# Kernel optimization log

Hardware: AMD Instinct MI355X
Metric: run time of the kernel (lower is better)

## Reference

```python
import jax, jax.numpy as jnp
import numpy as np

PADDED_NODE_ID = -1


def setup_inputs() -> dict:
    key = jax.random.key(0)
    k0, k1, k2, k3 = jax.random.split(key, 4)
    B, N, F = 1024, 512, 64
    src_ids = jax.random.randint(k0, (B, N), 0, 1000, dtype=jnp.int64 if jax.config.jax_enable_x64 else jnp.int32)
    dst_ids = jax.random.randint(k1, (B, N), 0, 1000, dtype=src_ids.dtype)
    W1 = jax.random.normal(k2, (1, F), dtype=jnp.float32) * 0.1   # Linear(1 -> F)
    b1 = jnp.zeros((F,), dtype=jnp.float32)
    W2 = jax.random.normal(k3, (F, F), dtype=jnp.float32) * 0.05  # Linear(F -> F)
    b2 = jnp.zeros((F,), dtype=jnp.float32)
    return {"src_ids": src_ids, "dst_ids": dst_ids, "W1": W1, "b1": b1, "W2": W2, "b2": b2}


def _count_freqs(src_ids, dst_ids):
    # For each row, count occurrences of each neighbor id within its own row
    # and within the paired row (cross-lookup). Equivalent to np.unique counts
    # plus dict-based cross mapping in the original, vectorized as pairwise
    # equality reductions over [B, N, N].
    def eq_count(a, b):
        return (a[:, :, None] == b[:, None, :]).sum(-1).astype(jnp.float32)  # [B, N]

    src_in_src = eq_count(src_ids, src_ids)
    src_in_dst = eq_count(src_ids, dst_ids)
    dst_in_dst = eq_count(dst_ids, dst_ids)
    dst_in_src = eq_count(dst_ids, src_ids)

    source_freq = jnp.stack([src_in_src, src_in_dst], axis=-1)  # [B, N, 2]
    dst_freq = jnp.stack([dst_in_dst, dst_in_src], axis=-1)     # [B, N, 2]

    # zero out padded positions
    source_freq = jnp.where((src_ids == PADDED_NODE_ID)[..., None], 0.0, source_freq)
    dst_freq = jnp.where((dst_ids == PADDED_NODE_ID)[..., None], 0.0, dst_freq)
    return source_freq, dst_freq


def reference(src_ids, dst_ids, W1, b1, W2, b2):
    source_freq, dst_freq = _count_freqs(src_ids, dst_ids)  # [B, N, 2] each

    def encode(freq):
        # freq[..., None] has shape [B, N, 2, 1]; Linear(1->F) is an outer product
        h = jax.nn.relu(freq[..., None] * W1[0] + b1)        # [B, N, 2, F]
        h = jnp.einsum('bnkf,fg->bnkg', h, W2) + b2          # [B, N, 2, F]
        return h.sum(axis=2)                                 # [B, N, F]

    return encode(source_freq), encode(dst_freq)
```

## Files before the change

### kernel.cpp

```cpp
#include <hip/hip_runtime.h>

#define BATCH 1024
#define NSEQ  512
#define NF    64
#define TBL_N (NSEQ + 1)
#define HIST_BINS 1024

#define TBL_BLOCKS ((TBL_N + 3) / 4)

__global__ __launch_bounds__(256) void build_table_kernel(
        const float* __restrict__ W1,
        const float* __restrict__ b1,
        const float* __restrict__ W2,
        const float* __restrict__ b2,
        float* __restrict__ tbl) {
    const int c = blockIdx.x * 4 + (threadIdx.x >> 6);
    const int g = threadIdx.x & 63;
    if (c >= TBL_N) return;
    const float cf = (float)c;
    float acc = b2[g];
#pragma unroll 8
    for (int f = 0; f < NF; ++f) {
        float h = fmaxf(cf * W1[f] + b1[f], 0.0f);
        acc += h * W2[f * NF + g];
    }
    tbl[c * NF + g] = acc;
}

__global__ __launch_bounds__(256) void expand_kernel(
        const int* __restrict__ src_ids,
        const int* __restrict__ dst_ids,
        const float* __restrict__ tbl,
        float* __restrict__ out) {
    __shared__ int     s_src[NSEQ];
    __shared__ int     s_dst[NSEQ];
    __shared__ int     hist_s[HIST_BINS];
    __shared__ int     hist_d[HIST_BINS];
    __shared__ ushort2 s_cnt[NSEQ];

    const int t     = threadIdx.x;
    const int which = blockIdx.x & 1;
    const int row   = blockIdx.x >> 1;

#pragma unroll
    for (int i = t; i < HIST_BINS; i += 256) { hist_s[i] = 0; hist_d[i] = 0; }
#pragma unroll
    for (int i = t; i < NSEQ; i += 256) {
        s_src[i] = src_ids[(size_t)row * NSEQ + i];
        s_dst[i] = dst_ids[(size_t)row * NSEQ + i];
    }
    __syncthreads();

#pragma unroll
    for (int i = t; i < NSEQ; i += 256) {
        int si = s_src[i], di = s_dst[i];
        if (si >= 0) atomicAdd(&hist_s[si], 1);
        if (di >= 0) atomicAdd(&hist_d[di], 1);
    }
    __syncthreads();

#pragma unroll
    for (int i = t; i < NSEQ; i += 256) {
        int id = (which == 0) ? s_src[i] : s_dst[i];
        ushort2 c;
        if (id >= 0) {
            c.x = (unsigned short)((which == 0) ? hist_s[id] : hist_d[id]);
            c.y = (unsigned short)((which == 0) ? hist_d[id] : hist_s[id]);
        } else {
            c.x = 0; c.y = 0;
        }
        s_cnt[i] = c;
    }
    __syncthreads();

    const float4* __restrict__ tbl4 = (const float4*)tbl;
    float4* __restrict__ o = (float4*)(out + ((size_t)which * BATCH + row) * NSEQ * NF);
    const int NV = NSEQ * NF / 4;
#pragma unroll 8
    for (int e = t; e < NV; e += 256) {
        int n  = e >> 4;
        int f4 = e & 15;
        ushort2 c = s_cnt[n];
        float4 a0 = tbl4[((int)c.x << 4) + f4];
        float4 a1 = tbl4[((int)c.y << 4) + f4];
        o[e] = make_float4(a0.x + a1.x, a0.y + a1.y, a0.z + a1.z, a0.w + a1.w);
    }
}

extern "C" void kernel_launch(void* const* d_in, const int* in_sizes, int n_in,
                              void* d_out, int out_size, void* d_ws, size_t ws_size,
                              hipStream_t stream) {
    const int*   src_ids = (const int*)d_in[0];
    const int*   dst_ids = (const int*)d_in[1];
    const float* W1 = (const float*)d_in[2];
    const float* b1 = (const float*)d_in[3];
    const float* W2 = (const float*)d_in[4];
    const float* b2 = (const float*)d_in[5];

    float* out = (float*)d_out;
    float* tbl = (float*)d_ws;

    build_table_kernel<<<TBL_BLOCKS, 256, 0, stream>>>(W1, b1, W2, b2, tbl);
    expand_kernel<<<2 * BATCH, 256, 0, stream>>>(src_ids, dst_ids, tbl, out);
}
```

Baseline: 51.32 us.

## Fuse table build into expand kernel with per-block hot table in shared memory

Removes the separate table-building kernel. Each block instead computes a small table for counts below 16 in shared memory and writes outputs from it. Pairs with larger counts fall back to a non-inlined function that computes the MLP directly. This saves a launch and global table reads, but every block now repeats the small table computation and a divergent slow path is added.

```diff
diff --git a/kernel.cpp b/kernel.cpp
--- a/kernel.cpp
+++ b/kernel.cpp
@@ -3,40 +3,42 @@
 #define BATCH 1024
 #define NSEQ  512
 #define NF    64
-#define TBL_N (NSEQ + 1)
 #define HIST_BINS 1024
 
-#define TBL_BLOCKS ((TBL_N + 3) / 4)
+#define HOT 16
+#define TSTRIDE 68
 
-__global__ __launch_bounds__(256) void build_table_kernel(
+__device__ __noinline__ float4 cold_pair(int c0, int c1, int f4,
+                                         const float* __restrict__ W1,
+                                         const float* __restrict__ b1,
+                                         const float* __restrict__ W2,
+                                         const float* __restrict__ b2) {
+    const int g0 = 4 * f4;
+    float a0 = 2.0f * b2[g0 + 0], a1 = 2.0f * b2[g0 + 1];
+    float a2 = 2.0f * b2[g0 + 2], a3 = 2.0f * b2[g0 + 3];
+    for (int f = 0; f < NF; ++f) {
+        float w = W1[f], b = b1[f];
+        float hs = fmaxf((float)c0 * w + b, 0.0f) + fmaxf((float)c1 * w + b, 0.0f);
+        const float* w2 = &W2[f * NF + g0];
+        a0 += hs * w2[0]; a1 += hs * w2[1]; a2 += hs * w2[2]; a3 += hs * w2[3];
+    }
+    return make_float4(a0, a1, a2, a3);
+}
+
+__global__ __launch_bounds__(256, 4) void fused_expand_kernel(
+        const int* __restrict__ src_ids,
+        const int* __restrict__ dst_ids,
         const float* __restrict__ W1,
         const float* __restrict__ b1,
         const float* __restrict__ W2,
         const float* __restrict__ b2,
-        float* __restrict__ tbl) {
-    const int c = blockIdx.x * 4 + (threadIdx.x >> 6);
-    const int g = threadIdx.x & 63;
-    if (c >= TBL_N) return;
-    const float cf = (float)c;
-    float acc = b2[g];
-#pragma unroll 8
-    for (int f = 0; f < NF; ++f) {
-        float h = fmaxf(cf * W1[f] + b1[f], 0.0f);
-        acc += h * W2[f * NF + g];
-    }
-    tbl[c * NF + g] = acc;
-}
-
-__global__ __launch_bounds__(256) void expand_kernel(
-        const int* __restrict__ src_ids,
-        const int* __restrict__ dst_ids,
-        const float* __restrict__ tbl,
         float* __restrict__ out) {
     __shared__ int     s_src[NSEQ];
     __shared__ int     s_dst[NSEQ];
     __shared__ int     hist_s[HIST_BINS];
     __shared__ int     hist_d[HIST_BINS];
     __shared__ ushort2 s_cnt[NSEQ];
+    __shared__ float   s_tbl[HOT * TSTRIDE];
 
     const int t     = threadIdx.x;
     const int which = blockIdx.x & 1;
@@ -48,6 +50,19 @@
     for (int i = t; i < NSEQ; i += 256) {
         s_src[i] = src_ids[(size_t)row * NSEQ + i];
         s_dst[i] = dst_ids[(size_t)row * NSEQ + i];
+    }
+#pragma unroll
+    for (int k = 0; k < (HOT * NF) / 256; ++k) {
+        const int idx = t + k * 256;
+        const int r = idx >> 6, g = idx & 63;
+        const float cf = (float)r;
+        float acc = b2[g];
+#pragma unroll 8
+        for (int f = 0; f < NF; ++f) {
+            float h = fmaxf(cf * W1[f] + b1[f], 0.0f);
+            acc += h * W2[f * NF + g];
+        }
+        s_tbl[r * TSTRIDE + g] = acc;
     }
     __syncthreads();
 
@@ -64,8 +79,10 @@
         int id = (which == 0) ? s_src[i] : s_dst[i];
         ushort2 c;
         if (id >= 0) {
-            c.x = (unsigned short)((which == 0) ? hist_s[id] : hist_d[id]);
-            c.y = (unsigned short)((which == 0) ? hist_d[id] : hist_s[id]);
+            int own   = (which == 0) ? hist_s[id] : hist_d[id];
+            int cross = (which == 0) ? hist_d[id] : hist_s[id];
+            c.x = (unsigned short)own;
+            c.y = (unsigned short)cross;
         } else {
             c.x = 0; c.y = 0;
         }
@@ -73,17 +90,22 @@
     }
     __syncthreads();
 
-    const float4* __restrict__ tbl4 = (const float4*)tbl;
     float4* __restrict__ o = (float4*)(out + ((size_t)which * BATCH + row) * NSEQ * NF);
     const int NV = NSEQ * NF / 4;
 #pragma unroll 8
     for (int e = t; e < NV; e += 256) {
-        int n  = e >> 4;
-        int f4 = e & 15;
-        ushort2 c = s_cnt[n];
-        float4 a0 = tbl4[((int)c.x << 4) + f4];
-        float4 a1 = tbl4[((int)c.y << 4) + f4];
-        o[e] = make_float4(a0.x + a1.x, a0.y + a1.y, a0.z + a1.z, a0.w + a1.w);
+        const int n  = e >> 4;
+        const int f4 = e & 15;
+        const ushort2 c = s_cnt[n];
+        float4 r;
+        if (((int)c.x | (int)c.y) < HOT) {
+            const float4 a0 = *(const float4*)&s_tbl[(int)c.x * TSTRIDE + 4 * f4];
+            const float4 a1 = *(const float4*)&s_tbl[(int)c.y * TSTRIDE + 4 * f4];
+            r = make_float4(a0.x + a1.x, a0.y + a1.y, a0.z + a1.z, a0.w + a1.w);
+        } else {
+            r = cold_pair((int)c.x, (int)c.y, f4, W1, b1, W2, b2);
+        }
+        o[e] = r;
     }
 }
 
@@ -98,8 +120,7 @@
     const float* b2 = (const float*)d_in[5];
 
     float* out = (float*)d_out;
-    float* tbl = (float*)d_ws;
 
-    build_table_kernel<<<TBL_BLOCKS, 256, 0, stream>>>(W1, b1, W2, b2, tbl);
-    expand_kernel<<<2 * BATCH, 256, 0, stream>>>(src_ids, dst_ids, tbl, out);
+    fused_expand_kernel<<<2 * BATCH, 256, 0, stream>>>(
+        src_ids, dst_ids, W1, b1, W2, b2, out);
 }
```

Measured after the change: 57.60 us. +12.2%, slower.

## Cache hot count rows of lookup table in LDS with global overflow fallback

Applied to the files above, without the earlier changes.

The expand kernel now copies the first 32 rows of the precomputed count-to-feature table into shared memory and does its gather from LDS using precomputed byte offsets. Positions whose own or cross count reaches 32 are recorded in an overflow list and rewritten afterwards from the global table. It also drops the shared copies of the id rows and rereads ids from global memory. The goal is to cut L2/global gather traffic in the output-bound expansion loop, at the cost of a per-block table preload, an extra barrier and a rarely taken fixup pass.

```diff
diff --git a/kernel.cpp b/kernel.cpp
--- a/kernel.cpp
+++ b/kernel.cpp
@@ -6,6 +6,7 @@
 #define TBL_N (NSEQ + 1)
 #define HIST_BINS 1024
 
+#define HOT 32
 #define TBL_BLOCKS ((TBL_N + 3) / 4)
 
 __global__ __launch_bounds__(256) void build_table_kernel(
@@ -30,30 +31,37 @@
 __global__ __launch_bounds__(256) void expand_kernel(
         const int* __restrict__ src_ids,
         const int* __restrict__ dst_ids,
-        const float* __restrict__ tbl,
+        const float* __restrict__ g_tbl,
         float* __restrict__ out) {
-    __shared__ int     s_src[NSEQ];
-    __shared__ int     s_dst[NSEQ];
-    __shared__ int     hist_s[HIST_BINS];
-    __shared__ int     hist_d[HIST_BINS];
-    __shared__ ushort2 s_cnt[NSEQ];
+    __shared__ int            hist_s[HIST_BINS];
+    __shared__ int            hist_d[HIST_BINS];
+    __shared__ float          s_tbl[HOT * NF];
+    __shared__ ushort2        s_off[NSEQ];
+    __shared__ unsigned short s_ovf[NSEQ];
+    __shared__ int            s_novf;
 
     const int t     = threadIdx.x;
     const int which = blockIdx.x & 1;
     const int row   = blockIdx.x >> 1;
 
+    const int* __restrict__ own_ids = (which == 0) ? src_ids : dst_ids;
+
 #pragma unroll
     for (int i = t; i < HIST_BINS; i += 256) { hist_s[i] = 0; hist_d[i] = 0; }
+    if (t == 0) s_novf = 0;
+
+    {
+        const float4* __restrict__ g4 = (const float4*)g_tbl;
+        float4* __restrict__ l4 = (float4*)s_tbl;
 #pragma unroll
-    for (int i = t; i < NSEQ; i += 256) {
-        s_src[i] = src_ids[(size_t)row * NSEQ + i];
-        s_dst[i] = dst_ids[(size_t)row * NSEQ + i];
+        for (int i = t; i < HOT * NF / 4; i += 256) l4[i] = g4[i];
     }
     __syncthreads();
 
 #pragma unroll
     for (int i = t; i < NSEQ; i += 256) {
-        int si = s_src[i], di = s_dst[i];
+        int si = src_ids[(size_t)row * NSEQ + i];
+        int di = dst_ids[(size_t)row * NSEQ + i];
         if (si >= 0) atomicAdd(&hist_s[si], 1);
         if (di >= 0) atomicAdd(&hist_d[di], 1);
     }
@@ -61,29 +69,54 @@
 
 #pragma unroll
     for (int i = t; i < NSEQ; i += 256) {
-        int id = (which == 0) ? s_src[i] : s_dst[i];
-        ushort2 c;
+        int id = own_ids[(size_t)row * NSEQ + i];
+        int own = 0, cross = 0;
         if (id >= 0) {
-            c.x = (unsigned short)((which == 0) ? hist_s[id] : hist_d[id]);
-            c.y = (unsigned short)((which == 0) ? hist_d[id] : hist_s[id]);
-        } else {
-            c.x = 0; c.y = 0;
+            own   = (which == 0) ? hist_s[id] : hist_d[id];
+            cross = (which == 0) ? hist_d[id] : hist_s[id];
         }
-        s_cnt[i] = c;
+        if (own >= HOT || cross >= HOT) {
+            int k = atomicAdd(&s_novf, 1);
+            s_ovf[k] = (unsigned short)i;
+        }
+        ushort2 off;
+        off.x = (unsigned short)(min(own,   HOT - 1) * (NF * 4));
+        off.y = (unsigned short)(min(cross, HOT - 1) * (NF * 4));
+        s_off[i] = off;
     }
     __syncthreads();
 
-    const float4* __restrict__ tbl4 = (const float4*)tbl;
     float4* __restrict__ o = (float4*)(out + ((size_t)which * BATCH + row) * NSEQ * NF);
+    const char* __restrict__ tb = (const char*)s_tbl;
     const int NV = NSEQ * NF / 4;
-#pragma unroll 8
+#pragma unroll 4
     for (int e = t; e < NV; e += 256) {
-        int n  = e >> 4;
-        int f4 = e & 15;
-        ushort2 c = s_cnt[n];
-        float4 a0 = tbl4[((int)c.x << 4) + f4];
-        float4 a1 = tbl4[((int)c.y << 4) + f4];
+        const int n  = e >> 4;
+        const int fb = (e & 15) << 4;
+        const ushort2 c = s_off[n];
+        const float4 a0 = *(const float4*)(tb + (int)c.x + fb);
+        const float4 a1 = *(const float4*)(tb + (int)c.y + fb);
         o[e] = make_float4(a0.x + a1.x, a0.y + a1.y, a0.z + a1.z, a0.w + a1.w);
+    }
+
+    __syncthreads();
+    const int novf = s_novf;
+    if (novf > 0) {
+        const float4* __restrict__ g4 = (const float4*)g_tbl;
+        for (int k = t >> 4; k < novf; k += 16) {
+            const int i  = s_ovf[k];
+            const int f4 = t & 15;
+            const int id = own_ids[(size_t)row * NSEQ + i];
+            int own = 0, cross = 0;
+            if (id >= 0) {
+                own   = (which == 0) ? hist_s[id] : hist_d[id];
+                cross = (which == 0) ? hist_d[id] : hist_s[id];
+            }
+            float4 a0 = g4[own * (NF / 4) + f4];
+            float4 a1 = g4[cross * (NF / 4) + f4];
+            o[i * 16 + f4] = make_float4(a0.x + a1.x, a0.y + a1.y,
+                                         a0.z + a1.z, a0.w + a1.w);
+        }
     }
 }
 
```

New measurement: 50.99 us. Within noise of the previous version (-0.6%).
